# Kernel tuning notes

Measured on AMD Instinct MI355X. Metric: run time of the kernel, lower is better.

Reference implementation:

```python
import jax, jax.numpy as jnp
import numpy as np

WEIGHT_SCALE = 0.01      # weight_scale buffer
WEIGHT_ZP = 8            # weight_zero_point buffer
BIAS_SCALE = 0.01 * 0.047  # bias_scale = weight_scale * activation_scale (from_float)
OUT_FEATURES = 4096
IN_FEATURES = 4096


def setup_inputs() -> dict:
    key = jax.random.key(0)
    k1, k2, k3 = jax.random.split(key, 3)
    x = jax.random.normal(k1, (8, 2048, IN_FEATURES), dtype=jnp.float32)
    # packed uint8 bytes, two 4-bit weights per byte; stored as int32 (values 0..255)
    packed_weight = jax.random.randint(k2, (OUT_FEATURES, IN_FEATURES // 2), 0, 256, dtype=jnp.int32)
    quantized_bias = jax.random.randint(k3, (OUT_FEATURES,), -500, 500, dtype=jnp.int32)
    return {"x": x, "packed_weight": packed_weight, "quantized_bias": quantized_bias}


def _dequantize_weights(packed_weight):
    # low nibble -> even input column, high nibble -> odd input column
    low = packed_weight & 15          # [O, I/2]
    high = (packed_weight >> 4) & 15  # [O, I/2]
    q = jnp.stack([low, high], axis=-1).reshape(OUT_FEATURES, IN_FEATURES)
    return WEIGHT_SCALE * (q.astype(jnp.float32) - WEIGHT_ZP)


def reference(x, packed_weight, quantized_bias):
    W = _dequantize_weights(packed_weight)                 # [O, I]
    b = BIAS_SCALE * quantized_bias.astype(jnp.float32)    # [O]
    # F.linear: x @ W.T + b
    return jnp.einsum('bsi,oi->bso', x, W) + b
```

## Files before the change

### kernel.cpp

```cpp
#include <hip/hip_runtime.h>


typedef __bf16 bf16x8 __attribute__((ext_vector_type(8)));
typedef float f32x4 __attribute__((ext_vector_type(4)));
typedef unsigned short u16;
typedef u16 u16x4 __attribute__((ext_vector_type(4)));
typedef u16 u16x8 __attribute__((ext_vector_type(8)));

static constexpr int Kdim = 4096;
static constexpr int Ndim = 4096;
static constexpr int BM = 256, BN = 256, BK = 32;
static constexpr int NKT = Kdim / BK;
static constexpr int BUFH = BM * BK;

__device__ __forceinline__ u16 f2bf(float f) {
  union { float f; unsigned u; } c; c.f = f;
  unsigned u = c.u;
  return (u16)((u + 0x7FFFu + ((u >> 16) & 1u)) >> 16);
}

__global__ __launch_bounds__(256) void cvt_x_kernel(const float* __restrict__ x,
                                                    u16* __restrict__ xb, int n4) {
  int stride = gridDim.x * blockDim.x;
  for (int i = blockIdx.x * blockDim.x + threadIdx.x; i < n4; i += stride) {
    float4 v = reinterpret_cast<const float4*>(x)[i];
    u16x4 o;
    o.x = f2bf(v.x); o.y = f2bf(v.y); o.z = f2bf(v.z); o.w = f2bf(v.w);
    reinterpret_cast<u16x4*>(xb)[i] = o;
  }
}

__global__ __launch_bounds__(256) void dequant_w_kernel(const int* __restrict__ pw,
                                                        u16* __restrict__ wb, int n4) {
  int stride = gridDim.x * blockDim.x;
  for (int i = blockIdx.x * blockDim.x + threadIdx.x; i < n4; i += stride) {
    int4 v = reinterpret_cast<const int4*>(pw)[i];
    int a[4] = {v.x, v.y, v.z, v.w};
    u16x8 o;
#pragma unroll
    for (int j = 0; j < 4; ++j) {
      o[2 * j]     = f2bf((float)((a[j] & 15) - 8));
      o[2 * j + 1] = f2bf((float)(((a[j] >> 4) & 15) - 8));
    }
    reinterpret_cast<u16x8*>(wb)[i] = o;
  }
}

__device__ __forceinline__ void gload16(const u16* g, const u16* l) {
  __builtin_amdgcn_global_load_lds(
      (const __attribute__((address_space(1))) void*)g,
      (__attribute__((address_space(3))) void*)l,
      16, 0, 0);
}

__global__ __launch_bounds__(512, 2) void gemm_kernel(const u16* __restrict__ A,
                                                      const u16* __restrict__ B,
                                                      const int* __restrict__ qbias,
                                                      float* __restrict__ C,
                                                      int Mtiles) {
  extern __shared__ u16 smem[];
  u16* As = smem;
  u16* Bs = smem + 4 * BUFH;

  const int tid = threadIdx.x;
  const int wave = tid >> 6, lane = tid & 63;
  const int wm = wave >> 2, wn = wave & 3;

  const int nwg = gridDim.x;
  const int cpx = nwg >> 3;
  const int bid = blockIdx.x;
  const int swz = (bid & 7) * cpx + (bid >> 3);
  const int by = swz % Mtiles;
  const int bx = swz / Mtiles;
  const int m0 = by * BM, n0 = bx * BN;

  const int c0 = tid, c1 = 512 + tid;
  const int r0 = c0 >> 2, r1 = c1 >> 2;
  const int f0 = ((c0 & 3) ^ (r0 & 3)) << 3;
  const int f1 = ((c1 & 3) ^ (r1 & 3)) << 3;
  const u16* pa0 = A + (size_t)(m0 + r0) * Kdim + f0;
  const u16* pa1 = A + (size_t)(m0 + r1) * Kdim + f1;
  const u16* pb0 = B + (size_t)(n0 + r0) * Kdim + f0;
  const u16* pb1 = B + (size_t)(n0 + r1) * Kdim + f1;
  const int ldsc0 = (0 * 512 + (tid & 0x1C0)) * 8;
  const int ldsc1 = (1 * 512 + (tid & 0x1C0)) * 8;

  const int rA = wm * 128 + (lane & 15);
  const int rB = wn * 64 + (lane & 15);
  const int kof = ((lane >> 4) ^ (lane & 3)) << 3;

  f32x4 acc[8][4] = {};

#pragma unroll
  for (int tt = 0; tt < 3; ++tt) {
    const int ko = tt * BK;
    const u16* la = As + tt * BUFH;
    const u16* lb = Bs + tt * BUFH;
    gload16(pa0 + ko, la + ldsc0);
    gload16(pa1 + ko, la + ldsc1);
    gload16(pb0 + ko, lb + ldsc0);
    gload16(pb1 + ko, lb + ldsc1);
  }
  asm volatile("s_waitcnt vmcnt(8)" ::: "memory");
  __builtin_amdgcn_s_barrier();

  for (int t = 0; t < NKT; ++t) {
    const u16* a_lds = As + (t & 3) * BUFH;
    const u16* b_lds = Bs + (t & 3) * BUFH;
    const u16* a_wr = As + ((t + 3) & 3) * BUFH;
    const u16* b_wr = Bs + ((t + 3) & 3) * BUFH;
    const bool st = (t + 3) < NKT;
    const int ko = (t + 3) * BK;

    bf16x8 alo[4], bfr[4];
#pragma unroll
    for (int m = 0; m < 4; ++m)
      alo[m] = *(const bf16x8*)(a_lds + (rA + m * 16) * BK + kof);
#pragma unroll
    for (int n = 0; n < 4; ++n)
      bfr[n] = *(const bf16x8*)(b_lds + (rB + n * 16) * BK + kof);
    if (st) { gload16(pa0 + ko, a_wr + ldsc0); gload16(pa1 + ko, a_wr + ldsc1); }
    __builtin_amdgcn_s_barrier();
    asm volatile("s_waitcnt lgkmcnt(0)" ::: "memory");
    __builtin_amdgcn_sched_barrier(0);
    __builtin_amdgcn_s_setprio(1);
#pragma unroll
    for (int m = 0; m < 4; ++m)
#pragma unroll
      for (int n = 0; n < 4; ++n)
        acc[m][n] = __builtin_amdgcn_mfma_f32_16x16x32_bf16(alo[m], bfr[n], acc[m][n], 0, 0, 0);
    __builtin_amdgcn_s_setprio(0);
    __builtin_amdgcn_sched_barrier(0);
    __builtin_amdgcn_s_barrier();

    bf16x8 ahi[4];
#pragma unroll
    for (int m = 0; m < 4; ++m)
      ahi[m] = *(const bf16x8*)(a_lds + (rA + 64 + m * 16) * BK + kof);
    if (st) { gload16(pb0 + ko, b_wr + ldsc0); gload16(pb1 + ko, b_wr + ldsc1); }
    __builtin_amdgcn_s_barrier();
    asm volatile("s_waitcnt lgkmcnt(0)" ::: "memory");
    __builtin_amdgcn_sched_barrier(0);
    __builtin_amdgcn_s_setprio(1);
#pragma unroll
    for (int m = 0; m < 4; ++m)
#pragma unroll
      for (int n = 0; n < 4; ++n)
        acc[m + 4][n] = __builtin_amdgcn_mfma_f32_16x16x32_bf16(ahi[m], bfr[n], acc[m + 4][n], 0, 0, 0);
    __builtin_amdgcn_s_setprio(0);
    __builtin_amdgcn_sched_barrier(0);

    if (t + 3 < NKT)      asm volatile("s_waitcnt vmcnt(8)" ::: "memory");
    else if (t + 2 < NKT) asm volatile("s_waitcnt vmcnt(4)" ::: "memory");
    else if (t + 1 < NKT) asm volatile("s_waitcnt vmcnt(0)" ::: "memory");
    __builtin_amdgcn_s_barrier();
  }

  const float wscale = 0.01f;
  const float bscale = (float)(0.01 * 0.047);
  const int col0 = n0 + wn * 64 + (lane & 15);
  const int row0 = m0 + wm * 128 + ((lane >> 4) << 2);
#pragma unroll
  for (int n = 0; n < 4; ++n) {
    const int col = col0 + n * 16;
    const float bias = bscale * (float)qbias[col];
#pragma unroll
    for (int m = 0; m < 8; ++m) {
      const int rr = row0 + m * 16;
#pragma unroll
      for (int j = 0; j < 4; ++j)
        C[(size_t)(rr + j) * Ndim + col] = wscale * acc[m][n][j] + bias;
    }
  }
}

extern "C" void kernel_launch(void* const* d_in, const int* in_sizes, int n_in,
                              void* d_out, int out_size, void* d_ws, size_t ws_size,
                              hipStream_t stream) {
  const float* x  = (const float*)d_in[0];
  const int*   pw = (const int*)d_in[1];
  const int*   qb = (const int*)d_in[2];
  float* out = (float*)d_out;

  const int M = in_sizes[0] / Kdim;

  u16* xb = (u16*)d_ws;
  u16* wb = (u16*)((char*)d_ws + (size_t)M * Kdim * 2);

  cvt_x_kernel<<<2048, 256, 0, stream>>>(x, xb, M * Kdim / 4);
  dequant_w_kernel<<<1024, 256, 0, stream>>>(pw, wb, Ndim * Kdim / 8);

  const int Mtiles = M / BM;
  const int nwg = Mtiles * (Ndim / BN);
  static const size_t lds_bytes = 2u * 4u * BUFH * sizeof(u16);
  (void)hipFuncSetAttribute((const void*)gemm_kernel,
                            hipFuncAttributeMaxDynamicSharedMemorySize,
                            (int)lds_bytes);
  gemm_kernel<<<nwg, 512, lds_bytes, stream>>>(xb, wb, qb, out, Mtiles);
}
```

Before: 640.3 us.

## Retile GEMM to 256x128x64 with triple-buffered LDS and 4x2 wave grid

Changes the block tile from 256x256x32 to 256x128x64 and arranges the 8 waves as 4x2, each computing a 64x64 subtile with a 4x4 accumulator array instead of 8x4. The LDS pipeline moves from 4 buffers of depth-3 prefetch to 3 buffers with depth-2 prefetch, using an 8-way XOR swizzle for the wider K slice. This halves accumulator registers per wave and doubles the workgroup count, which may improve occupancy and load balance. The cost is lower arithmetic intensity per tile because each tile reuses the A data over fewer columns, and prefetch depth is shallower.

```diff
diff --git a/kernel.cpp b/kernel.cpp
--- a/kernel.cpp
+++ b/kernel.cpp
@@ -9,9 +9,10 @@
 
 static constexpr int Kdim = 4096;
 static constexpr int Ndim = 4096;
-static constexpr int BM = 256, BN = 256, BK = 32;
+static constexpr int BM = 256, BN = 128, BK = 64;
 static constexpr int NKT = Kdim / BK;
-static constexpr int BUFH = BM * BK;
+static constexpr int ABUF = BM * BK;
+static constexpr int BBUF = BN * BK;
 
 __device__ __forceinline__ u16 f2bf(float f) {
   union { float f; unsigned u; } c; c.f = f;
@@ -60,66 +61,74 @@
                                                       int Mtiles) {
   extern __shared__ u16 smem[];
   u16* As = smem;
-  u16* Bs = smem + 4 * BUFH;
+  u16* Bs = smem + 3 * ABUF;
 
   const int tid = threadIdx.x;
-  const int wave = tid >> 6, lane = tid & 63;
-  const int wm = wave >> 2, wn = wave & 3;
-
-  const int nwg = gridDim.x;
-  const int cpx = nwg >> 3;
+  const int lane = tid & 63;
+  const int wave = tid >> 6;
+  const int wm = wave >> 1, wn = wave & 1;
+
+  const int cpx = gridDim.x >> 3;
   const int bid = blockIdx.x;
   const int swz = (bid & 7) * cpx + (bid >> 3);
   const int by = swz % Mtiles;
   const int bx = swz / Mtiles;
   const int m0 = by * BM, n0 = bx * BN;
 
-  const int c0 = tid, c1 = 512 + tid;
-  const int r0 = c0 >> 2, r1 = c1 >> 2;
-  const int f0 = ((c0 & 3) ^ (r0 & 3)) << 3;
-  const int f1 = ((c1 & 3) ^ (r1 & 3)) << 3;
-  const u16* pa0 = A + (size_t)(m0 + r0) * Kdim + f0;
-  const u16* pa1 = A + (size_t)(m0 + r1) * Kdim + f1;
-  const u16* pb0 = B + (size_t)(n0 + r0) * Kdim + f0;
-  const u16* pb1 = B + (size_t)(n0 + r1) * Kdim + f1;
-  const int ldsc0 = (0 * 512 + (tid & 0x1C0)) * 8;
-  const int ldsc1 = (1 * 512 + (tid & 0x1C0)) * 8;
-
-  const int rA = wm * 128 + (lane & 15);
-  const int rB = wn * 64 + (lane & 15);
-  const int kof = ((lane >> 4) ^ (lane & 3)) << 3;
-
-  f32x4 acc[8][4] = {};
-
-#pragma unroll
-  for (int tt = 0; tt < 3; ++tt) {
+  const int srow = tid >> 3;
+  const int fcol = (((tid & 7) ^ (srow & 7)) << 3);
+  const u16* pa[4];
+#pragma unroll
+  for (int i = 0; i < 4; ++i)
+    pa[i] = A + (size_t)(m0 + i * 64 + srow) * Kdim + fcol;
+  const u16* pb[2];
+#pragma unroll
+  for (int i = 0; i < 2; ++i)
+    pb[i] = B + (size_t)(n0 + i * 64 + srow) * Kdim + fcol;
+  const int wbase = (tid & 0x1C0) * 8;
+
+  const int rowh = lane & 15;
+  const int e0 = ((lane >> 4) ^ (lane & 7)) << 3;
+  const int e1 = e0 ^ 32;
+  const int aoff = (wm * 64 + rowh) * 64;
+  const int boff = (wn * 64 + rowh) * 64;
+
+  f32x4 acc[4][4] = {};
+
+#pragma unroll
+  for (int tt = 0; tt < 2; ++tt) {
+    const u16* aW = As + tt * ABUF;
+    const u16* bW = Bs + tt * BBUF;
     const int ko = tt * BK;
-    const u16* la = As + tt * BUFH;
-    const u16* lb = Bs + tt * BUFH;
-    gload16(pa0 + ko, la + ldsc0);
-    gload16(pa1 + ko, la + ldsc1);
-    gload16(pb0 + ko, lb + ldsc0);
-    gload16(pb1 + ko, lb + ldsc1);
-  }
-  asm volatile("s_waitcnt vmcnt(8)" ::: "memory");
+#pragma unroll
+    for (int i = 0; i < 4; ++i) gload16(pa[i] + ko, aW + i * 4096 + wbase);
+#pragma unroll
+    for (int i = 0; i < 2; ++i) gload16(pb[i] + ko, bW + i * 4096 + wbase);
+  }
+  asm volatile("s_waitcnt vmcnt(6)" ::: "memory");
   __builtin_amdgcn_s_barrier();
 
+  int rbuf = 0, wbuf = 2;
   for (int t = 0; t < NKT; ++t) {
-    const u16* a_lds = As + (t & 3) * BUFH;
-    const u16* b_lds = Bs + (t & 3) * BUFH;
-    const u16* a_wr = As + ((t + 3) & 3) * BUFH;
-    const u16* b_wr = Bs + ((t + 3) & 3) * BUFH;
-    const bool st = (t + 3) < NKT;
-    const int ko = (t + 3) * BK;
-
-    bf16x8 alo[4], bfr[4];
-#pragma unroll
-    for (int m = 0; m < 4; ++m)
-      alo[m] = *(const bf16x8*)(a_lds + (rA + m * 16) * BK + kof);
+    const u16* aL = As + rbuf * ABUF;
+    const u16* bL = Bs + rbuf * BBUF;
+    const u16* aW = As + wbuf * ABUF;
+    const u16* bW = Bs + wbuf * BBUF;
+    const bool st = (t + 2) < NKT;
+    const int ko = (t + 2) * BK;
+
+    bf16x8 af[4], bf[4];
+#pragma unroll
+    for (int m = 0; m < 4; ++m)
+      af[m] = *(const bf16x8*)(aL + aoff + m * 1024 + e0);
 #pragma unroll
     for (int n = 0; n < 4; ++n)
-      bfr[n] = *(const bf16x8*)(b_lds + (rB + n * 16) * BK + kof);
-    if (st) { gload16(pa0 + ko, a_wr + ldsc0); gload16(pa1 + ko, a_wr + ldsc1); }
+      bf[n] = *(const bf16x8*)(bL + boff + n * 1024 + e0);
+    if (st) {
+      gload16(pa[0] + ko, aW + 0 * 4096 + wbase);
+      gload16(pa[1] + ko, aW + 1 * 4096 + wbase);
+      gload16(pa[2] + ko, aW + 2 * 4096 + wbase);
+    }
     __builtin_amdgcn_s_barrier();
     asm volatile("s_waitcnt lgkmcnt(0)" ::: "memory");
     __builtin_amdgcn_sched_barrier(0);
@@ -128,16 +137,22 @@
     for (int m = 0; m < 4; ++m)
 #pragma unroll
       for (int n = 0; n < 4; ++n)
-        acc[m][n] = __builtin_amdgcn_mfma_f32_16x16x32_bf16(alo[m], bfr[n], acc[m][n], 0, 0, 0);
+        acc[m][n] = __builtin_amdgcn_mfma_f32_16x16x32_bf16(af[m], bf[n], acc[m][n], 0, 0, 0);
     __builtin_amdgcn_s_setprio(0);
     __builtin_amdgcn_sched_barrier(0);
     __builtin_amdgcn_s_barrier();
 
-    bf16x8 ahi[4];
-#pragma unroll
-    for (int m = 0; m < 4; ++m)
-      ahi[m] = *(const bf16x8*)(a_lds + (rA + 64 + m * 16) * BK + kof);
-    if (st) { gload16(pb0 + ko, b_wr + ldsc0); gload16(pb1 + ko, b_wr + ldsc1); }
+#pragma unroll
+    for (int m = 0; m < 4; ++m)
+      af[m] = *(const bf16x8*)(aL + aoff + m * 1024 + e1);
+#pragma unroll
+    for (int n = 0; n < 4; ++n)
+      bf[n] = *(const bf16x8*)(bL + boff + n * 1024 + e1);
+    if (st) {
+      gload16(pa[3] + ko, aW + 3 * 4096 + wbase);
+      gload16(pb[0] + ko, bW + 0 * 4096 + wbase);
+      gload16(pb[1] + ko, bW + 1 * 4096 + wbase);
+    }
     __builtin_amdgcn_s_barrier();
     asm volatile("s_waitcnt lgkmcnt(0)" ::: "memory");
     __builtin_amdgcn_sched_barrier(0);
@@ -146,26 +161,28 @@
     for (int m = 0; m < 4; ++m)
 #pragma unroll
       for (int n = 0; n < 4; ++n)
-        acc[m + 4][n] = __builtin_amdgcn_mfma_f32_16x16x32_bf16(ahi[m], bfr[n], acc[m + 4][n], 0, 0, 0);
+        acc[m][n] = __builtin_amdgcn_mfma_f32_16x16x32_bf16(af[m], bf[n], acc[m][n], 0, 0, 0);
     __builtin_amdgcn_s_setprio(0);
     __builtin_amdgcn_sched_barrier(0);
 
-    if (t + 3 < NKT)      asm volatile("s_waitcnt vmcnt(8)" ::: "memory");
-    else if (t + 2 < NKT) asm volatile("s_waitcnt vmcnt(4)" ::: "memory");
+    if (t + 2 < NKT)      asm volatile("s_waitcnt vmcnt(6)" ::: "memory");
     else if (t + 1 < NKT) asm volatile("s_waitcnt vmcnt(0)" ::: "memory");
     __builtin_amdgcn_s_barrier();
+
+    rbuf = (rbuf == 2) ? 0 : rbuf + 1;
+    wbuf = (wbuf == 2) ? 0 : wbuf + 1;
   }
 
   const float wscale = 0.01f;
   const float bscale = (float)(0.01 * 0.047);
   const int col0 = n0 + wn * 64 + (lane & 15);
-  const int row0 = m0 + wm * 128 + ((lane >> 4) << 2);
+  const int row0 = m0 + wm * 64 + ((lane >> 4) << 2);
 #pragma unroll
   for (int n = 0; n < 4; ++n) {
     const int col = col0 + n * 16;
     const float bias = bscale * (float)qbias[col];
 #pragma unroll
-    for (int m = 0; m < 8; ++m) {
+    for (int m = 0; m < 4; ++m) {
       const int rr = row0 + m * 16;
 #pragma unroll
       for (int j = 0; j < 4; ++j)
@@ -192,7 +209,7 @@
 
   const int Mtiles = M / BM;
   const int nwg = Mtiles * (Ndim / BN);
-  static const size_t lds_bytes = 2u * 4u * BUFH * sizeof(u16);
+  static const size_t lds_bytes = (3u * ABUF + 3u * BBUF) * sizeof(u16);
   (void)hipFuncSetAttribute((const void*)gemm_kernel,
                             hipFuncAttributeMaxDynamicSharedMemorySize,
                             (int)lds_bytes);
```

Measured after the change: 755.9 us. 18.1% more time.
